# Performance work log

Measured on AMD Instinct MI355X. Metric: run time of the kernel, lower is better.

## Reference

```python
import jax, jax.numpy as jnp
import numpy as np

# Model dims (match init_kwargs)
B, S = 2, 2048
H = 1024          # hidden_size
I = 256           # intermediate_size
E = 256           # n_routed_experts
K = 8             # num_experts_per_tok
G = 8             # n_group
TG = 4            # topk_group
NS = 2            # n_shared_experts


def setup_inputs() -> dict:
    key = jax.random.key(0)
    ks = jax.random.split(key, 6)
    s = 0.02
    return {
        "x": jax.random.normal(ks[0], (B, S, H), jnp.float32),
        "Wg": jax.random.normal(ks[1], (E, H), jnp.float32) * s,          # gate Linear weight [E,H] (y = x @ Wg.T)
        "W_gate_up": jax.random.normal(ks[2], (E, H, 2 * I), jnp.float32) * s,  # per-expert gate_up proj
        "W_down": jax.random.normal(ks[3], (E, I, H), jnp.float32) * s,          # per-expert down proj
        "Ws_gate_up": jax.random.normal(ks[4], (NS, H, 2 * I), jnp.float32) * s, # shared experts
        "Ws_down": jax.random.normal(ks[5], (NS, I, H), jnp.float32) * s,
    }


def _mlp(x, w_gu, w_d):
    # DeepSeekV3 MLP: down( silu(gate) * up ); gate/up are the two chunks of gate_up
    gu = x @ w_gu                      # [N, 2I]
    g, u = gu[..., :I], gu[..., I:]
    return (jax.nn.silu(g) * u) @ w_d  # [N, H]


def reference(x, Wg, W_gate_up, W_down, Ws_gate_up, Ws_down):
    b, s, h = x.shape
    xf = x.reshape(-1, h)              # [N, H]
    n = xf.shape[0]

    # ---- shared experts (always active, averaged) ----
    shared = (_mlp(xf, Ws_gate_up[0], Ws_down[0]) + _mlp(xf, Ws_gate_up[1], Ws_down[1])) / NS

    # ---- grouped top-k gating ----
    logits = xf @ Wg.T                               # [N, E]
    gsize = E // G
    gl = logits.reshape(n, G, gsize)                 # [N, G, gsize]
    g_top_l, g_top_i = jax.lax.top_k(gl, TG)         # top-TG within each group
    cand_l = g_top_l.reshape(n, G * TG)              # candidate logits (group-major)
    cand_i = g_top_i.reshape(n, G * TG)              # within-group expert ids
    top_l, pos = jax.lax.top_k(cand_l, K)            # global top-K over candidates
    topk_idx = (pos // TG) * gsize + jnp.take_along_axis(cand_i, pos, axis=1)  # [N, K]
    topk_w = jax.nn.softmax(top_l, axis=-1)          # [N, K]

    # ---- routed experts: sort-by-expert + grouped GEMM (ragged_dot) ----
    flat_idx = topk_idx.reshape(-1)                  # [N*K]
    flat_w = topk_w.reshape(-1)
    order = jnp.argsort(flat_idx)                    # tokens grouped by expert id
    tok = order // K                                 # source token of each assignment
    xs = xf[tok]                                     # [N*K, H] gathered tokens, expert-contiguous
    gsz = jnp.bincount(flat_idx, length=E).astype(jnp.int32)  # tokens per expert

    gu = jax.lax.ragged_dot(xs, W_gate_up, gsz)      # [N*K, 2I] grouped GEMM 1
    hmid = jax.nn.silu(gu[:, :I]) * gu[:, I:]
    yo = jax.lax.ragged_dot(hmid, W_down, gsz)       # [N*K, H] grouped GEMM 2
    yo = yo * flat_w[order][:, None]                 # weight by gate prob

    routed = jnp.zeros_like(xf).at[tok].add(yo)      # scatter-add combine

    return (shared + routed).reshape(b, s, h)
```

## Files before the change

### kernel.cpp

```cpp
#include <hip/hip_runtime.h>
#include <hip/hip_bf16.h>


typedef __attribute__((ext_vector_type(4))) float  f32x4;
typedef __attribute__((ext_vector_type(8))) short  bf16x8;
typedef __attribute__((ext_vector_type(4))) short  bf16x4;
typedef __attribute__((ext_vector_type(4))) unsigned short u16x4;

#define DI static __device__ __forceinline__

DI unsigned short f2bf(float f){
  unsigned u = __builtin_bit_cast(unsigned, f);
  return (unsigned short)((u + 0x7FFFu + ((u>>16)&1u)) >> 16);
}
DI float bf2f(unsigned short s){
  return __builtin_bit_cast(float, ((unsigned)s)<<16);
}

#define WS_XBF      0u
#define WS_HSH      8388608u
#define WS_HMID     12582912u
#define WS_YSLOT    29360128u
#define WS_WGT      29360128u
#define WS_TOPKI    96468992u
#define WS_TOPKW    96600064u
#define WS_TOKMAP   96731136u
#define WS_SLOTMAP  96862208u
#define WS_CNT      96993280u
#define WS_CURSOR   96994304u
#define WS_ZERO     96995328u
#define WS_OFF      96999424u

__global__ __launch_bounds__(256) void k_wgT(const float* __restrict__ Wg, float* __restrict__ WgT){
  __shared__ float t[64][65];
  const int tid = threadIdx.x;
  const int hx = blockIdx.x * 64;
  const int ex = blockIdx.y * 64;
  #pragma unroll
  for (int k=0;k<16;++k){
    int i = (tid>>6)*16 + k, j = tid&63;
    t[i][j] = Wg[(size_t)(ex+i)*1024 + hx + j];
  }
  __syncthreads();
  #pragma unroll
  for (int k=0;k<16;++k){
    int i = (tid>>6)*16 + k, j = tid&63;
    WgT[(size_t)(hx+i)*256 + ex + j] = t[j][i];
  }
}

__global__ __launch_bounds__(256) void k_router(const float* __restrict__ x, const float* __restrict__ WgT,
                                                unsigned short* __restrict__ xbf,
                                                int* __restrict__ topki, float* __restrict__ topkw,
                                                int* __restrict__ cnt){
  __shared__ float xs[8][1024];
  __shared__ float lg[8][256];
  __shared__ float cv[8][32];
  __shared__ int   ce[8][32];
  const int tid = threadIdx.x;
  const int t0  = blockIdx.x * 8;
  {
    const f32x4* xg = (const f32x4*)(x + (size_t)t0*1024);
    f32x4* xs4 = (f32x4*)&xs[0][0];
    u16x4* xb4 = (u16x4*)(xbf + (size_t)t0*1024);
    #pragma unroll
    for (int i=0;i<8;++i){
      f32x4 v = xg[tid + i*256];
      xs4[tid + i*256] = v;
      u16x4 p; p[0]=f2bf(v[0]); p[1]=f2bf(v[1]); p[2]=f2bf(v[2]); p[3]=f2bf(v[3]);
      xb4[tid + i*256] = p;
    }
  }
  __syncthreads();
  {
    f32x4 a4[8];
    #pragma unroll
    for (int t=0;t<8;++t) a4[t] = (f32x4){0.f,0.f,0.f,0.f};
    const float* wc = WgT + tid;
    for (int h4=0; h4<256; ++h4){
      float w0 = wc[(size_t)(h4*4+0)*256];
      float w1 = wc[(size_t)(h4*4+1)*256];
      float w2 = wc[(size_t)(h4*4+2)*256];
      float w3 = wc[(size_t)(h4*4+3)*256];
      f32x4 wv = (f32x4){w0,w1,w2,w3};
      #pragma unroll
      for (int t=0;t<8;++t){
        f32x4 xv = *((const f32x4*)&xs[t][0] + h4);
        a4[t] += wv * xv;
      }
    }
    #pragma unroll
    for (int t=0;t<8;++t){
      double d = ((double)a4[t][0] + (double)a4[t][1]) + ((double)a4[t][2] + (double)a4[t][3]);
      lg[t][tid] = (float)d;
    }
  }
  __syncthreads();
  if (tid < 64){
    int tok = tid>>3, grp = tid&7;
    unsigned mask = 0;
    for (int j=0;j<4;++j){
      float best = -3.4e38f; int bi = 0;
      for (int i=0;i<32;++i){
        float v = lg[tok][grp*32+i];
        if (!((mask>>i)&1u) && v > best){ best=v; bi=i; }
      }
      mask |= 1u<<bi;
      cv[tok][grp*4+j] = best; ce[tok][grp*4+j] = grp*32+bi;
    }
  }
  __syncthreads();
  if (tid < 8){
    int tok = tid; unsigned mask=0;
    float vals[8]; int es[8];
    #pragma unroll
    for (int k=0;k<8;++k){
      float best=-3.4e38f; int bp=0;
      for (int p=0;p<32;++p){
        float v = cv[tok][p];
        if (!((mask>>p)&1u) && v > best){ best=v; bp=p; }
      }
      mask|=1u<<bp; vals[k]=best; es[k]=ce[tok][bp];
    }
    float m = vals[0], s=0.f, w[8];
    #pragma unroll
    for (int k=0;k<8;++k){ w[k]=expf(vals[k]-m); s+=w[k]; }
    float inv = 1.f/s;
    #pragma unroll
    for (int k=0;k<8;++k){
      int g=(t0+tok)*8+k;
      topki[g]=es[k]; topkw[g]=w[k]*inv;
      atomicAdd(&cnt[es[k]],1);
    }
  }
}

__global__ void k_scan(const int* __restrict__ cnt, int* __restrict__ off){
  __shared__ int s[256];
  int tid=threadIdx.x;
  s[tid]=cnt[tid]; __syncthreads();
  for (int d=1; d<256; d<<=1){
    int v = (tid>=d)? s[tid-d] : 0; __syncthreads();
    s[tid]+=v; __syncthreads();
  }
  off[tid+1]=s[tid]; if(tid==0) off[0]=0;
}

__global__ void k_scatter(const int* __restrict__ topki, const int* __restrict__ off,
                          int* __restrict__ cursor, int* __restrict__ tokmap, int* __restrict__ slotmap){
  int g = blockIdx.x*256 + threadIdx.x;
  int e = topki[g];
  int p = off[e] + atomicAdd(&cursor[e], 1);
  tokmap[p] = g >> 3;
  slotmap[g] = p;
}

template<int GEMM>
__global__ __launch_bounds__(512, 4) void k_gemm(
    const unsigned short* __restrict__ A1, const unsigned short* __restrict__ A2,
    const float* __restrict__ WE, const float* __restrict__ WS,
    const int* __restrict__ cnt, const int* __restrict__ off,
    const int* __restrict__ tokmap,
    unsigned short* __restrict__ O1, unsigned short* __restrict__ O2,
    float* __restrict__ OD, const unsigned short* __restrict__ zpage)
{
  __shared__ __align__(16) char smem[65536];
  const int bx = blockIdx.x, mt = blockIdx.y, nc = blockIdx.z;
  const bool sh = (bx >= 256);
  int e = bx, s = 0, M, Moff;
  if (!sh){ M = cnt[e]; Moff = mt*256; }
  else {
    int sidx = bx - 256;
    if (GEMM==1){ s = sidx>>3; Moff = (sidx&7)*512 + mt*256; }
    else        { s = 0;       Moff = sidx*512 + mt*256; }
    M = 4096;
  }
  if (Moff >= M) return;
  const int tid=threadIdx.x, ln=tid&63, wv=tid>>6, wm=wv>>2, wn=wv&3, lrow=ln&15, lk=ln>>4;
  const int Ktot = (GEMM==1)?1024:(sh?512:256);
  const int ldB  = (GEMM==1)?512:1024;
  const float* Bp = (GEMM==1) ? (sh? WS + (size_t)s*524288 : WE + (size_t)e*524288)
                              : (sh? WS : WE + (size_t)e*262144);
  const int offe = sh? 0 : off[e];

  const char* a_src[2];
  #pragma unroll
  for (int qi=0;qi<2;++qi){
    int row  = (wv*2+qi)*16 + (ln>>2);
    int grow = Moff + row;
    const unsigned short* p;
    if (GEMM==1){
      if (!sh) p = (grow < M)? A1 + (size_t)tokmap[offe+grow]*1024 : zpage;
      else     p = A1 + (size_t)grow*1024;
    } else {
      if (!sh) p = (grow < M)? A1 + ((size_t)offe+grow)*256 : zpage;
      else     p = A2 + (size_t)grow*512;
    }
    a_src[qi] = (const char*)p + (ln&3)*16;
  }
  const char* b_src[2];
  {
    int swz = ((wv>>1)&3)<<2;
    int cg  = (ln&31) ^ swz;
    int c4  = cg*4;
    int gcol = (GEMM==1) ? ((c4<64)? nc*64 + c4 : 256 + nc*64 + (c4-64))
                         : (nc*128 + c4);
    int rbase = 4*wv + (ln>>5);
    #pragma unroll
    for (int q=0;q<2;++q)
      b_src[q] = (const char*)(Bp + (size_t)(rbase + 2*q)*ldB + gcol);
  }

  f32x4 acc[8][2] = {};

  auto stage = [&](int buf, int k0){
    #pragma unroll
    for (int qi=0;qi<2;++qi)
      __builtin_amdgcn_global_load_lds((const void*)(a_src[qi] + (size_t)k0*2),
          (void*)(smem + buf*16384 + (wv*2+qi)*1024), 16, 0, 0);
    #pragma unroll
    for (int q=0;q<2;++q)
      __builtin_amdgcn_global_load_lds((const void*)(b_src[q] + (size_t)k0*ldB*4),
          (void*)(smem + 32768 + buf*16384 + wv*2048 + q*1024), 16, 0, 0);
  };

  auto compute = [&](int buf){
    const short* as  = (const short*)(smem + buf*16384);
    const float* bs  = (const float*)(smem + 32768 + buf*16384);
    bf16x8 bv[2];
    #pragma unroll
    for (int ni=0;ni<2;++ni){
      int tc = (GEMM==1)? (ni*64 + wn*16 + lrow) : (wn*32 + ni*16 + lrow);
      int sloff = ((((tc>>2) ^ (lk<<2))<<2) | (tc&3));
      const float* colp = bs + (size_t)lk*8*128 + sloff;
      #pragma unroll
      for (int j=0;j<8;++j){
        unsigned u = __builtin_bit_cast(unsigned, colp[(size_t)j*128]);
        bv[ni][j] = (short)((u + 0x8000u) >> 16);
      }
    }
    #pragma unroll
    for (int mi=0;mi<8;++mi){
      if (Moff + wm*128 + mi*16 < M){
        bf16x8 af = *(const bf16x8*)(as + (wm*128+mi*16+lrow)*32 + lk*8);
        acc[mi][0] = __builtin_amdgcn_mfma_f32_16x16x32_bf16(af, bv[0], acc[mi][0], 0,0,0);
        acc[mi][1] = __builtin_amdgcn_mfma_f32_16x16x32_bf16(af, bv[1], acc[mi][1], 0,0,0);
      }
    }
  };

  stage(0, 0);
  const int ns = Ktot>>5;
  for (int t=0;t<ns;++t){
    int b = t&1;
    if (t+1<ns){
      stage(b^1, (t+1)<<5);
      asm volatile("s_waitcnt vmcnt(4)" ::: "memory");
    } else {
      asm volatile("s_waitcnt vmcnt(0)" ::: "memory");
    }
    asm volatile("s_barrier" ::: "memory");
    compute(b);
    asm volatile("s_barrier" ::: "memory");
  }

  if (GEMM==1){
    __syncthreads();
    unsigned short* Hs = (unsigned short*)smem;
    #pragma unroll
    for (int mi=0;mi<8;++mi){
      f32x4 g = acc[mi][0], u = acc[mi][1];
      #pragma unroll
      for (int r=0;r<4;++r){
        float gg = g[r];
        float hh = (gg / (1.f + __expf(-gg))) * u[r];
        int m = wm*128 + mi*16 + lk*4 + r;
        Hs[m*72 + wn*16 + lrow] = f2bf(hh);
      }
    }
    __syncthreads();
    #pragma unroll
    for (int i=0;i<4;++i){
      int id = tid + i*512, m = id>>3, c8 = id&7;
      int grow = Moff + m;
      if (grow < M){
        unsigned short* dst = (!sh) ? O1 + ((size_t)offe + grow)*256 + nc*64 + c8*8
                                    : O2 + (size_t)grow*512 + (size_t)s*256 + nc*64 + c8*8;
        *(f32x4*)dst = *(const f32x4*)(Hs + m*72 + c8*8);
      }
    }
  } else {
    if (sh){
      #pragma unroll
      for (int mi=0;mi<8;++mi)
        #pragma unroll
        for (int ni=0;ni<2;++ni)
          #pragma unroll
          for (int r=0;r<4;++r){
            int m = Moff + wm*128 + mi*16 + lk*4 + r;
            int c = nc*128 + wn*32 + ni*16 + lrow;
            OD[(size_t)m*1024 + c] = acc[mi][ni][r]*0.5f;
          }
    } else {
      __syncthreads();
      unsigned short* Hs = (unsigned short*)smem;
      #pragma unroll
      for (int mi=0;mi<8;++mi)
        #pragma unroll
        for (int ni=0;ni<2;++ni)
          #pragma unroll
          for (int r=0;r<4;++r){
            int m = wm*128 + mi*16 + lk*4 + r;
            int c = wn*32 + ni*16 + lrow;
            Hs[m*128 + c] = f2bf(acc[mi][ni][r]);
          }
      __syncthreads();
      #pragma unroll
      for (int i=0;i<8;++i){
        int id = tid + i*512, m = id>>4, c8 = id&15;
        int grow = Moff + m;
        if (grow < M){
          unsigned short* dst = O1 + ((size_t)offe+grow)*1024 + nc*128 + c8*8;
          *(f32x4*)dst = *(const f32x4*)(Hs + m*128 + c8*8);
        }
      }
    }
  }
}

__global__ void k_final(float* __restrict__ out, const unsigned short* __restrict__ yslot,
                        const int* __restrict__ slotmap, const float* __restrict__ topkw){
  __shared__ int sp[8]; __shared__ float sw[8];
  int t = blockIdx.x, tid = threadIdx.x;
  if (tid<8){ sp[tid]=slotmap[t*8+tid]; sw[tid]=topkw[t*8+tid]; }
  __syncthreads();
  int c = tid*4;
  f32x4 o = *(f32x4*)(out + (size_t)t*1024 + c);
  #pragma unroll
  for (int k=0;k<8;++k){
    u16x4 y = *(const u16x4*)(yslot + (size_t)sp[k]*1024 + c);
    float w = sw[k];
    o[0] += w*bf2f(y[0]); o[1] += w*bf2f(y[1]); o[2] += w*bf2f(y[2]); o[3] += w*bf2f(y[3]);
  }
  *(f32x4*)(out + (size_t)t*1024 + c) = o;
}

extern "C" void kernel_launch(void* const* d_in, const int* in_sizes, int n_in,
                              void* d_out, int out_size, void* d_ws, size_t ws_size,
                              hipStream_t stream) {
  const float* x    = (const float*)d_in[0];
  const float* Wg   = (const float*)d_in[1];
  const float* Wgu  = (const float*)d_in[2];
  const float* Wd   = (const float*)d_in[3];
  const float* Wsgu = (const float*)d_in[4];
  const float* Wsd  = (const float*)d_in[5];
  float* out = (float*)d_out;

  char* W = (char*)d_ws;
  unsigned short* xbf    = (unsigned short*)(W + WS_XBF);
  unsigned short* hsh    = (unsigned short*)(W + WS_HSH);
  unsigned short* hmid   = (unsigned short*)(W + WS_HMID);
  unsigned short* yslot  = (unsigned short*)(W + WS_YSLOT);
  float* WgT     = (float*)(W + WS_WGT);
  int*   topki   = (int*)(W + WS_TOPKI);
  float* topkw   = (float*)(W + WS_TOPKW);
  int*   tokmap  = (int*)(W + WS_TOKMAP);
  int*   slotmap = (int*)(W + WS_SLOTMAP);
  int*   cnt     = (int*)(W + WS_CNT);
  int*   cursor  = (int*)(W + WS_CURSOR);
  unsigned short* zpage = (unsigned short*)(W + WS_ZERO);
  int*   off     = (int*)(W + WS_OFF);

  hipMemsetAsync((void*)cnt, 0, 1024+1024+4096, stream);

  k_wgT    <<<dim3(16,4), 256, 0, stream>>>(Wg, WgT);
  k_router <<<512, 256, 0, stream>>>(x, WgT, xbf, topki, topkw, cnt);
  k_scan   <<<1, 256, 0, stream>>>(cnt, off);
  k_scatter<<<128, 256, 0, stream>>>(topki, off, cursor, tokmap, slotmap);
  k_gemm<1><<<dim3(272,2,4), 512, 0, stream>>>(xbf, (const unsigned short*)nullptr,
        Wgu, Wsgu, cnt, off, tokmap, hmid, hsh, out, zpage);
  k_gemm<2><<<dim3(264,2,8), 512, 0, stream>>>(hmid, hsh,
        Wd, Wsd, cnt, off, tokmap, yslot, (unsigned short*)nullptr, out, zpage);
  k_final <<<4096, 256, 0, stream>>>(out, yslot, slotmap, topkw);
}
```

Before: 354.2 us.

## Triple-buffer B tiles and skip A loads for empty rows in grouped GEMM

Splits the staging of A and B tiles, moves the B (fp32 weight) tiles to a three-stage ring buffer with prefetch distance two, and keeps A double-buffered. Waves whose A rows lie entirely past the expert's token count skip issuing A loads, using a compile-time specialised loop with adjusted vmcnt waits. This aims to hide more weight-load latency and to cut wasted global traffic on partially filled expert tiles. LDS grows from 64KB to 80KB per block, which may reduce occupancy under the 512-thread launch bounds.

```diff
diff --git a/kernel.cpp b/kernel.cpp
--- a/kernel.cpp
+++ b/kernel.cpp
@@ -8,6 +8,8 @@
 typedef __attribute__((ext_vector_type(4))) unsigned short u16x4;
 
 #define DI static __device__ __forceinline__
+
+template<bool B> struct BoolC { static constexpr bool value = B; };
 
 DI unsigned short f2bf(float f){
   unsigned u = __builtin_bit_cast(unsigned, f);
@@ -164,7 +166,7 @@
     unsigned short* __restrict__ O1, unsigned short* __restrict__ O2,
     float* __restrict__ OD, const unsigned short* __restrict__ zpage)
 {
-  __shared__ __align__(16) char smem[65536];
+  __shared__ __align__(16) char smem[81920];
   const int bx = blockIdx.x, mt = blockIdx.y, nc = blockIdx.z;
   const bool sh = (bx >= 256);
   int e = bx, s = 0, M, Moff;
@@ -213,20 +215,22 @@
 
   f32x4 acc[8][2] = {};
 
-  auto stage = [&](int buf, int k0){
+  auto stageA = [&](int buf, int k0){
     #pragma unroll
     for (int qi=0;qi<2;++qi)
       __builtin_amdgcn_global_load_lds((const void*)(a_src[qi] + (size_t)k0*2),
           (void*)(smem + buf*16384 + (wv*2+qi)*1024), 16, 0, 0);
+  };
+  auto stageB = [&](int buf, int k0){
     #pragma unroll
     for (int q=0;q<2;++q)
       __builtin_amdgcn_global_load_lds((const void*)(b_src[q] + (size_t)k0*ldB*4),
           (void*)(smem + 32768 + buf*16384 + wv*2048 + q*1024), 16, 0, 0);
   };
 
-  auto compute = [&](int buf){
-    const short* as  = (const short*)(smem + buf*16384);
-    const float* bs  = (const float*)(smem + 32768 + buf*16384);
+  auto compute = [&](int ab, int bb){
+    const short* as  = (const short*)(smem + ab*16384);
+    const float* bs  = (const float*)(smem + 32768 + bb*16384);
     bf16x8 bv[2];
     #pragma unroll
     for (int ni=0;ni<2;++ni){
@@ -249,20 +253,32 @@
     }
   };
 
-  stage(0, 0);
   const int ns = Ktot>>5;
-  for (int t=0;t<ns;++t){
-    int b = t&1;
-    if (t+1<ns){
-      stage(b^1, (t+1)<<5);
-      asm volatile("s_waitcnt vmcnt(4)" ::: "memory");
-    } else {
-      asm volatile("s_waitcnt vmcnt(0)" ::: "memory");
-    }
-    asm volatile("s_barrier" ::: "memory");
-    compute(b);
-    asm volatile("s_barrier" ::: "memory");
-  }
+  const bool skipA = (Moff + wv*32 >= M);
+
+  auto mainloop = [&](auto skc){
+    constexpr bool SK = decltype(skc)::value;
+    if constexpr (!SK) stageA(0, 0);
+    stageB(0, 0);
+    stageB(1, 32);
+    for (int t=0; t<ns; ++t){
+      if constexpr (!SK){ if (t+1<ns) stageA((t+1)&1, (t+1)<<5); }
+      if (t+2<ns) stageB((t+2)%3, (t+2)<<5);
+      if (t+2<ns){
+        if constexpr (SK) asm volatile("s_waitcnt vmcnt(4)" ::: "memory");
+        else              asm volatile("s_waitcnt vmcnt(6)" ::: "memory");
+      } else if (t+1<ns){
+        if constexpr (SK) asm volatile("s_waitcnt vmcnt(2)" ::: "memory");
+        else              asm volatile("s_waitcnt vmcnt(4)" ::: "memory");
+      } else {
+        asm volatile("s_waitcnt vmcnt(0)" ::: "memory");
+      }
+      asm volatile("s_barrier" ::: "memory");
+      compute(t&1, t%3);
+      asm volatile("s_barrier" ::: "memory");
+    }
+  };
+  if (skipA) mainloop(BoolC<true>{}); else mainloop(BoolC<false>{});
 
   if (GEMM==1){
     __syncthreads();
```

Result: no change. 357.9 us (+1.0%).

## Shrink grouped-GEMM M-tile to 128 rows with 4-wave blocks

Applied to the files above, without the earlier changes.

Each expert and shared-expert GEMM block now covers 128 rows with 256 threads (4 waves in a 2x2 layout) instead of 256 rows with 8 waves. Each wave computes a 64x64 sub-tile (4x4 MFMAs), the shared-memory buffers and staging offsets are resized, and the grid grows along y so more blocks cover the same work. The aim is to cut padding waste on experts with few tokens (about 128 on average) and raise the number of blocks in flight. In exchange, B-weight reuse per block drops, so more weight bytes are loaded and converted. Because gate and up columns now sit in different waves, the SiLU epilogue has to pass gate values through shared memory with extra barriers.

```diff
diff --git a/kernel.cpp b/kernel.cpp
--- a/kernel.cpp
+++ b/kernel.cpp
@@ -156,7 +156,7 @@
 }
 
 template<int GEMM>
-__global__ __launch_bounds__(512, 4) void k_gemm(
+__global__ __launch_bounds__(256, 3) void k_gemm(
     const unsigned short* __restrict__ A1, const unsigned short* __restrict__ A2,
     const float* __restrict__ WE, const float* __restrict__ WS,
     const int* __restrict__ cnt, const int* __restrict__ off,
@@ -164,19 +164,19 @@
     unsigned short* __restrict__ O1, unsigned short* __restrict__ O2,
     float* __restrict__ OD, const unsigned short* __restrict__ zpage)
 {
-  __shared__ __align__(16) char smem[65536];
+  __shared__ __align__(16) char smem[49152];
   const int bx = blockIdx.x, mt = blockIdx.y, nc = blockIdx.z;
   const bool sh = (bx >= 256);
   int e = bx, s = 0, M, Moff;
-  if (!sh){ M = cnt[e]; Moff = mt*256; }
+  if (!sh){ M = cnt[e]; Moff = mt*128; }
   else {
-    int sidx = bx - 256;
-    if (GEMM==1){ s = sidx>>3; Moff = (sidx&7)*512 + mt*256; }
-    else        { s = 0;       Moff = sidx*512 + mt*256; }
+    int idx = (bx-256)*4 + mt;
+    if (GEMM==1){ if (idx >= 64) return; s = idx>>5; Moff = (idx&31)*128; }
+    else        { if (idx >= 32) return; s = 0;      Moff = idx*128; }
     M = 4096;
   }
   if (Moff >= M) return;
-  const int tid=threadIdx.x, ln=tid&63, wv=tid>>6, wm=wv>>2, wn=wv&3, lrow=ln&15, lk=ln>>4;
+  const int tid=threadIdx.x, ln=tid&63, wv=tid>>6, wm=wv>>1, wn=wv&1, lrow=ln&15, lk=ln>>4;
   const int Ktot = (GEMM==1)?1024:(sh?512:256);
   const int ldB  = (GEMM==1)?512:1024;
   const float* Bp = (GEMM==1) ? (sh? WS + (size_t)s*524288 : WE + (size_t)e*524288)
@@ -198,39 +198,40 @@
     }
     a_src[qi] = (const char*)p + (ln&3)*16;
   }
-  const char* b_src[2];
+  const char* b_src[4];
   {
-    int swz = ((wv>>1)&3)<<2;
+    int swz = (wv&3)<<2;
     int cg  = (ln&31) ^ swz;
     int c4  = cg*4;
     int gcol = (GEMM==1) ? ((c4<64)? nc*64 + c4 : 256 + nc*64 + (c4-64))
                          : (nc*128 + c4);
-    int rbase = 4*wv + (ln>>5);
-    #pragma unroll
-    for (int q=0;q<2;++q)
-      b_src[q] = (const char*)(Bp + (size_t)(rbase + 2*q)*ldB + gcol);
-  }
-
-  f32x4 acc[8][2] = {};
+    #pragma unroll
+    for (int q=0;q<4;++q){
+      int kr = 8*wv + 2*q + (ln>>5);
+      b_src[q] = (const char*)(Bp + (size_t)kr*ldB + gcol);
+    }
+  }
+
+  f32x4 acc[4][4] = {};
 
   auto stage = [&](int buf, int k0){
     #pragma unroll
     for (int qi=0;qi<2;++qi)
       __builtin_amdgcn_global_load_lds((const void*)(a_src[qi] + (size_t)k0*2),
-          (void*)(smem + buf*16384 + (wv*2+qi)*1024), 16, 0, 0);
-    #pragma unroll
-    for (int q=0;q<2;++q)
+          (void*)(smem + buf*8192 + (wv*2+qi)*1024), 16, 0, 0);
+    #pragma unroll
+    for (int q=0;q<4;++q)
       __builtin_amdgcn_global_load_lds((const void*)(b_src[q] + (size_t)k0*ldB*4),
-          (void*)(smem + 32768 + buf*16384 + wv*2048 + q*1024), 16, 0, 0);
+          (void*)(smem + 16384 + buf*16384 + wv*4096 + q*1024), 16, 0, 0);
   };
 
   auto compute = [&](int buf){
-    const short* as  = (const short*)(smem + buf*16384);
-    const float* bs  = (const float*)(smem + 32768 + buf*16384);
-    bf16x8 bv[2];
-    #pragma unroll
-    for (int ni=0;ni<2;++ni){
-      int tc = (GEMM==1)? (ni*64 + wn*16 + lrow) : (wn*32 + ni*16 + lrow);
+    const short* as  = (const short*)(smem + buf*8192);
+    const float* bs  = (const float*)(smem + 16384 + buf*16384);
+    bf16x8 bv[4];
+    #pragma unroll
+    for (int ni=0;ni<4;++ni){
+      int tc = wn*64 + ni*16 + lrow;
       int sloff = ((((tc>>2) ^ (lk<<2))<<2) | (tc&3));
       const float* colp = bs + (size_t)lk*8*128 + sloff;
       #pragma unroll
@@ -240,11 +241,12 @@
       }
     }
     #pragma unroll
-    for (int mi=0;mi<8;++mi){
-      if (Moff + wm*128 + mi*16 < M){
-        bf16x8 af = *(const bf16x8*)(as + (wm*128+mi*16+lrow)*32 + lk*8);
-        acc[mi][0] = __builtin_amdgcn_mfma_f32_16x16x32_bf16(af, bv[0], acc[mi][0], 0,0,0);
-        acc[mi][1] = __builtin_amdgcn_mfma_f32_16x16x32_bf16(af, bv[1], acc[mi][1], 0,0,0);
+    for (int mi=0;mi<4;++mi){
+      if (Moff + wm*64 + mi*16 < M){
+        bf16x8 af = *(const bf16x8*)(as + (wm*64+mi*16+lrow)*32 + lk*8);
+        #pragma unroll
+        for (int ni=0;ni<4;++ni)
+          acc[mi][ni] = __builtin_amdgcn_mfma_f32_16x16x32_bf16(af, bv[ni], acc[mi][ni], 0,0,0);
       }
     }
   };
@@ -255,7 +257,7 @@
     int b = t&1;
     if (t+1<ns){
       stage(b^1, (t+1)<<5);
-      asm volatile("s_waitcnt vmcnt(4)" ::: "memory");
+      asm volatile("s_waitcnt vmcnt(6)" ::: "memory");
     } else {
       asm volatile("s_waitcnt vmcnt(0)" ::: "memory");
     }
@@ -266,58 +268,78 @@
 
   if (GEMM==1){
     __syncthreads();
-    unsigned short* Hs = (unsigned short*)smem;
-    #pragma unroll
-    for (int mi=0;mi<8;++mi){
-      f32x4 g = acc[mi][0], u = acc[mi][1];
-      #pragma unroll
-      for (int r=0;r<4;++r){
-        float gg = g[r];
-        float hh = (gg / (1.f + __expf(-gg))) * u[r];
-        int m = wm*128 + mi*16 + lk*4 + r;
-        Hs[m*72 + wn*16 + lrow] = f2bf(hh);
-      }
+    float* Hg = (float*)smem;
+    if (wn==0){
+      #pragma unroll
+      for (int mi=0;mi<4;++mi)
+        #pragma unroll
+        for (int ni=0;ni<4;++ni)
+          #pragma unroll
+          for (int r=0;r<4;++r)
+            Hg[(wm*64 + mi*16 + lk*4 + r)*64 + ni*16 + lrow] = acc[mi][ni][r];
     }
     __syncthreads();
+    unsigned short hv[4][4][4];
+    if (wn==1){
+      #pragma unroll
+      for (int mi=0;mi<4;++mi)
+        #pragma unroll
+        for (int ni=0;ni<4;++ni)
+          #pragma unroll
+          for (int r=0;r<4;++r){
+            float g = Hg[(wm*64 + mi*16 + lk*4 + r)*64 + ni*16 + lrow];
+            float hh = (g / (1.f + __expf(-g))) * acc[mi][ni][r];
+            hv[mi][ni][r] = f2bf(hh);
+          }
+    }
+    __syncthreads();
+    unsigned short* Hb = (unsigned short*)smem;
+    if (wn==1){
+      #pragma unroll
+      for (int mi=0;mi<4;++mi)
+        #pragma unroll
+        for (int ni=0;ni<4;++ni)
+          #pragma unroll
+          for (int r=0;r<4;++r)
+            Hb[(wm*64 + mi*16 + lk*4 + r)*72 + ni*16 + lrow] = hv[mi][ni][r];
+    }
+    __syncthreads();
     #pragma unroll
     for (int i=0;i<4;++i){
-      int id = tid + i*512, m = id>>3, c8 = id&7;
+      int id = tid + i*256, m = id>>3, c8 = id&7;
       int grow = Moff + m;
       if (grow < M){
         unsigned short* dst = (!sh) ? O1 + ((size_t)offe + grow)*256 + nc*64 + c8*8
                                     : O2 + (size_t)grow*512 + (size_t)s*256 + nc*64 + c8*8;
-        *(f32x4*)dst = *(const f32x4*)(Hs + m*72 + c8*8);
+        *(f32x4*)dst = *(const f32x4*)(Hb + m*72 + c8*8);
       }
     }
   } else {
     if (sh){
       #pragma unroll
-      for (int mi=0;mi<8;++mi)
-        #pragma unroll
-        for (int ni=0;ni<2;++ni)
+      for (int mi=0;mi<4;++mi)
+        #pragma unroll
+        for (int ni=0;ni<4;++ni)
           #pragma unroll
           for (int r=0;r<4;++r){
-            int m = Moff + wm*128 + mi*16 + lk*4 + r;
-            int c = nc*128 + wn*32 + ni*16 + lrow;
+            int m = Moff + wm*64 + mi*16 + lk*4 + r;
+            int c = nc*128 + wn*64 + ni*16 + lrow;
             OD[(size_t)m*1024 + c] = acc[mi][ni][r]*0.5f;
           }
     } else {
       __syncthreads();
       unsigned short* Hs = (unsigned short*)smem;
       #pragma unroll
-      for (int mi=0;mi<8;++mi)
-        #pragma unroll
-        for (int ni=0;ni<2;++ni)
+      for (int mi=0;mi<4;++mi)
+        #pragma unroll
+        for (int ni=0;ni<4;++ni)
           #pragma unroll
-          for (int r=0;r<4;++r){
-            int m = wm*128 + mi*16 + lk*4 + r;
-            int c = wn*32 + ni*16 + lrow;
-            Hs[m*128 + c] = f2bf(acc[mi][ni][r]);
-          }
+          for (int r=0;r<4;++r)
+            Hs[(wm*64 + mi*16 + lk*4 + r)*128 + wn*64 + ni*16 + lrow] = f2bf(acc[mi][ni][r]);
       __syncthreads();
       #pragma unroll
       for (int i=0;i<8;++i){
-        int id = tid + i*512, m = id>>4, c8 = id&15;
+        int id = tid + i*256, m = id>>4, c8 = id&15;
         int grow = Moff + m;
         if (grow < M){
           unsigned short* dst = O1 + ((size_t)offe+grow)*1024 + nc*128 + c8*8;
@@ -377,9 +399,9 @@
   k_router <<<512, 256, 0, stream>>>(x, WgT, xbf, topki, topkw, cnt);
   k_scan   <<<1, 256, 0, stream>>>(cnt, off);
   k_scatter<<<128, 256, 0, stream>>>(topki, off, cursor, tokmap, slotmap);
-  k_gemm<1><<<dim3(272,2,4), 512, 0, stream>>>(xbf, (const unsigned short*)nullptr,
+  k_gemm<1><<<dim3(320,4,4), 256, 0, stream>>>(xbf, (const unsigned short*)nullptr,
         Wgu, Wsgu, cnt, off, tokmap, hmid, hsh, out, zpage);
-  k_gemm<2><<<dim3(264,2,8), 512, 0, stream>>>(hmid, hsh,
+  k_gemm<2><<<dim3(264,4,8), 256, 0, stream>>>(hmid, hsh,
         Wd, Wsd, cnt, off, tokmap, yslot, (unsigned short*)nullptr, out, zpage);
   k_final <<<4096, 256, 0, stream>>>(out, yslot, slotmap, topkw);
 }
```

Result: slower. 395.7 us (+11.7%).
